# Kernel tuning notes

Measured on AMD Instinct MI355X. Metric: run time of the kernel, lower is better.

The kernel has to match this reference:

```python
import jax, jax.numpy as jnp
import numpy as np

N_NODES = 262144      # 2048 graphs * 128 nodes each
NUM_GRAPHS = 2048
MAX_NODES = 128
HIDDEN = 256
OUT_CH = 12
N_EDGES = 2097152     # ~avg degree 8


def setup_inputs() -> dict:
    key = jax.random.key(0)
    k1, k2, k3, k4 = jax.random.split(key, 4)
    x = jax.random.normal(k1, (N_NODES, HIDDEN), dtype=jnp.float32)
    # xavier-ish projection weight for Linear(6*hidden -> 12)
    W = jax.random.normal(k2, (OUT_CH, 6 * HIDDEN), dtype=jnp.float32) * (1.0 / np.sqrt(6 * HIDDEN))
    b = jnp.zeros((OUT_CH,), dtype=jnp.float32)
    # uniform graphs: sorted batch ids, MAX_NODES nodes per graph
    batch = (jnp.arange(N_NODES, dtype=jnp.int32) // MAX_NODES).astype(jnp.int32)
    # edges sampled within graphs: pick graph, then two local node ids
    g = jax.random.randint(k3, (N_EDGES,), 0, NUM_GRAPHS, dtype=jnp.int32)
    loc = jax.random.randint(k4, (N_EDGES, 2), 0, MAX_NODES, dtype=jnp.int32)
    src = g * MAX_NODES + loc[:, 0]
    dst = g * MAX_NODES + loc[:, 1]
    edge_index = jnp.stack([src, dst], axis=0).astype(jnp.int32)
    return {"x": x, "W": W, "b": b, "batch": batch, "edge_index": edge_index,
            "num_graphs": NUM_GRAPHS, "max_nodes": MAX_NODES}


def reference(x, W, b, batch, edge_index, num_graphs, max_nodes):
    N, H = x.shape
    G, M = num_graphs, max_nodes
    # local index of each node within its graph (batch is sorted by graph)
    counts = jax.ops.segment_sum(jnp.ones((N,), dtype=jnp.int32), batch, num_segments=G)
    starts = jnp.cumsum(counts) - counts            # exclusive prefix sum => first node of each graph
    local = jnp.arange(N, dtype=jnp.int32) - starts[batch]
    # dense per-graph node features X [G, M, H]
    X = jnp.zeros((G, M, H), dtype=x.dtype).at[batch, local].set(x)
    # dense symmetric adjacency A [G, M, M] (assignment semantics, like the torch loop)
    gi = batch[edge_index[0]]
    li = local[edge_index[0]]
    lj = local[edge_index[1]]
    A = jnp.zeros((G, M, M), dtype=x.dtype)
    A = A.at[gi, li, lj].set(1.0)
    A = A.at[gi, lj, li].set(1.0)
    # 6-gram walk readouts
    walk = X
    vs = [walk.sum(axis=1)]                          # v1
    for _ in range(5):                               # v2..v6
        walk = jnp.einsum('gnm,gmh->gnh', A, walk) * X
        vs.append(walk.sum(axis=1))
    out = jnp.concatenate(vs, axis=-1)               # == stack(dim=1).reshape(G, 6*H)
    out = out @ W.T + b                              # n_gram_projection
    return out
```

## Files before the change

### kernel.cpp

```cpp
#include <hip/hip_runtime.h>
#include <stdint.h>

#define NGRAPH 2048
#define MNODES 128
#define HID 256
#define OUTC 12
#define NEDGE 2097152

typedef __attribute__((ext_vector_type(8))) short short8;
typedef __attribute__((ext_vector_type(4))) float v4f;

#define SLICE 64
#define SWT_STRIDE 136

__device__ __forceinline__ unsigned short f2bf(float f) {
    unsigned int u = __builtin_bit_cast(unsigned int, f);
    u += 0x7fffu + ((u >> 16) & 1u);
    return (unsigned short)(u >> 16);
}

__global__ void build_bytes(const int* __restrict__ ei, unsigned char* __restrict__ Ab) {
    int e = blockIdx.x * blockDim.x + threadIdx.x;
    if (e >= NEDGE) return;
    int sN = ei[e];
    int dN = ei[NEDGE + e];
    int g = sN >> 7;
    int li = sN & 127;
    int lj = dN & 127;
    unsigned char* base = Ab + (size_t)g * (MNODES * MNODES);
    base[li * 128 + lj] = 1;
    base[lj * 128 + li] = 1;
}

__global__ void build_bits(const int* __restrict__ ei, unsigned int* __restrict__ bits) {
    int e = blockIdx.x * blockDim.x + threadIdx.x;
    if (e >= NEDGE) return;
    int sN = ei[e];
    int dN = ei[NEDGE + e];
    int g = sN >> 7;
    int li = sN & 127;
    int lj = dN & 127;
    unsigned int* base = bits + (size_t)g * (MNODES * 4);
    atomicOr(&base[li * 4 + (lj >> 5)], 1u << (lj & 31));
    atomicOr(&base[lj * 4 + (li >> 5)], 1u << (li & 31));
}

__launch_bounds__(256, 3)
__global__ void walk2(const float* __restrict__ x,
                      const float* __restrict__ W,
                      const unsigned char* __restrict__ Abytes,
                      const unsigned int* __restrict__ Abits,
                      int use_bytes,
                      float* __restrict__ partial) {
    __shared__ unsigned short sWT[SLICE][SWT_STRIDE];
    __shared__ float sVs2[2][6][SLICE];

    const int bx = blockIdx.x;
    const int g = bx >> 2;
    const int s = bx & 3;
    const int tid = threadIdx.x;
    const int wave = tid >> 6;
    const int lane = tid & 63;
    const int lrow = lane & 15;
    const int quad = lane >> 4;
    const int rhalf = wave >> 1;
    const int r0 = rhalf * 64;
    const int c0 = (wave & 1) * 32;
    const int cg0 = s * SLICE + c0;

    short8 areg[4][4];
    if (use_bytes) {
        const unsigned char* Ag = Abytes + (size_t)g * (MNODES * MNODES);
#pragma unroll
        for (int rt = 0; rt < 4; rt++) {
            int row = r0 + rt * 16 + lrow;
#pragma unroll
            for (int ks = 0; ks < 4; ks++) {
                int k0 = ks * 32 + quad * 8;
                uint2 u = *(const uint2*)(Ag + row * 128 + k0);
                short8 a;
#pragma unroll
                for (int j = 0; j < 8; j++) {
                    unsigned int byte = ((j < 4 ? u.x >> (8 * j) : u.y >> (8 * (j - 4))) & 0xFFu);
                    a[j] = (short)(byte ? 0x3F80 : 0);
                }
                areg[rt][ks] = a;
            }
        }
    } else {
        const unsigned int* Bg = Abits + (size_t)g * (MNODES * 4);
#pragma unroll
        for (int rt = 0; rt < 4; rt++) {
            int row = r0 + rt * 16 + lrow;
#pragma unroll
            for (int ks = 0; ks < 4; ks++) {
                unsigned int w = Bg[row * 4 + ks] >> (quad * 8);
                short8 a;
#pragma unroll
                for (int j = 0; j < 8; j++)
                    a[j] = (short)(((w >> j) & 1u) ? 0x3F80 : 0);
                areg[rt][ks] = a;
            }
        }
    }

    float xf[4][2][4];
    const float* xg = x + (size_t)g * (MNODES * HID);
#pragma unroll
    for (int rt = 0; rt < 4; rt++)
#pragma unroll
        for (int ct = 0; ct < 2; ct++) {
            int col = cg0 + ct * 16 + lrow;
#pragma unroll
            for (int reg = 0; reg < 4; reg++) {
                int row = r0 + rt * 16 + quad * 4 + reg;
                xf[rt][ct][reg] = xg[row * HID + col];
            }
        }
#pragma unroll
    for (int ct = 0; ct < 2; ct++) {
        int lcol = c0 + ct * 16 + lrow;
        float cs = 0.0f;
#pragma unroll
        for (int rt = 0; rt < 4; rt++) {
            int nbase = r0 + rt * 16 + quad * 4;
            uint2 u;
            u.x = (unsigned)f2bf(xf[rt][ct][0]) | ((unsigned)f2bf(xf[rt][ct][1]) << 16);
            u.y = (unsigned)f2bf(xf[rt][ct][2]) | ((unsigned)f2bf(xf[rt][ct][3]) << 16);
            *(uint2*)&sWT[lcol][nbase] = u;
            cs += xf[rt][ct][0] + xf[rt][ct][1] + xf[rt][ct][2] + xf[rt][ct][3];
        }
        cs += __shfl_xor(cs, 16);
        cs += __shfl_xor(cs, 32);
        if (quad == 0) sVs2[rhalf][0][lcol] = cs;
    }
    __syncthreads();

    for (int it = 1; it <= 5; it++) {
        v4f acc[4][2];
#pragma unroll
        for (int rt = 0; rt < 4; rt++)
#pragma unroll
            for (int ct = 0; ct < 2; ct++) acc[rt][ct] = (v4f)(0.0f);
#pragma unroll
        for (int ks = 0; ks < 4; ks++) {
            int k0 = ks * 32 + quad * 8;
#pragma unroll
            for (int ct = 0; ct < 2; ct++) {
                short8 bf = *(const short8*)&sWT[c0 + ct * 16 + lrow][k0];
#pragma unroll
                for (int rt = 0; rt < 4; rt++)
                    acc[rt][ct] = __builtin_amdgcn_mfma_f32_16x16x32_bf16(areg[rt][ks], bf, acc[rt][ct], 0, 0, 0);
            }
        }
        __syncthreads();
#pragma unroll
        for (int ct = 0; ct < 2; ct++) {
            int lcol = c0 + ct * 16 + lrow;
            float cs = 0.0f;
#pragma unroll
            for (int rt = 0; rt < 4; rt++) {
                float nw0 = acc[rt][ct][0] * xf[rt][ct][0];
                float nw1 = acc[rt][ct][1] * xf[rt][ct][1];
                float nw2 = acc[rt][ct][2] * xf[rt][ct][2];
                float nw3 = acc[rt][ct][3] * xf[rt][ct][3];
                int nbase = r0 + rt * 16 + quad * 4;
                uint2 u;
                u.x = (unsigned)f2bf(nw0) | ((unsigned)f2bf(nw1) << 16);
                u.y = (unsigned)f2bf(nw2) | ((unsigned)f2bf(nw3) << 16);
                *(uint2*)&sWT[lcol][nbase] = u;
                cs += nw0 + nw1 + nw2 + nw3;
            }
            cs += __shfl_xor(cs, 16);
            cs += __shfl_xor(cs, 32);
            if (quad == 0) sVs2[rhalf][it][lcol] = cs;
        }
        __syncthreads();
    }

    if (wave == 0) {
        for (int c = 0; c < OUTC; c++) {
            float p = 0.0f;
            const float* wr = W + c * (6 * HID);
#pragma unroll
            for (int ii = 0; ii < 6; ii++) {
                int i = ii * 64 + lane;
                int k = i >> 6;
                int h = i & 63;
                float v = sVs2[0][k][h] + sVs2[1][k][h];
                p += v * wr[k * HID + s * SLICE + h];
            }
#pragma unroll
            for (int off = 32; off >= 1; off >>= 1) p += __shfl_down(p, off);
            if (lane == 0) partial[bx * OUTC + c] = p;
        }
    }
}

__global__ void combine(const float* __restrict__ partial, const float* __restrict__ bvec,
                        float* __restrict__ out) {
    int i = blockIdx.x * blockDim.x + threadIdx.x;
    if (i >= NGRAPH * OUTC) return;
    int c = i % OUTC;
    int g = i / OUTC;
    float p = bvec[c];
#pragma unroll
    for (int s = 0; s < 4; s++) p += partial[(g * 4 + s) * OUTC + c];
    out[i] = p;
}

extern "C" void kernel_launch(void* const* d_in, const int* in_sizes, int n_in,
                              void* d_out, int out_size, void* d_ws, size_t ws_size,
                              hipStream_t stream) {
    const float* x = (const float*)d_in[0];
    const float* W = (const float*)d_in[1];
    const float* b = (const float*)d_in[2];
    const int* ei = (const int*)d_in[4];
    float* out = (float*)d_out;

    const size_t ABYTES = (size_t)NGRAPH * MNODES * MNODES;
    const size_t PARTIAL = (size_t)NGRAPH * 4 * OUTC * sizeof(float);

    if (ws_size >= ABYTES + PARTIAL) {
        unsigned char* Ab = (unsigned char*)d_ws;
        float* partial = (float*)((char*)d_ws + ABYTES);
        hipMemsetAsync(Ab, 0, ABYTES, stream);
        build_bytes<<<NEDGE / 256, 256, 0, stream>>>(ei, Ab);
        walk2<<<NGRAPH * 4, 256, 0, stream>>>(x, W, Ab, nullptr, 1, partial);
        combine<<<(NGRAPH * OUTC + 255) / 256, 256, 0, stream>>>(partial, b, out);
    } else {
        unsigned int* bits = (unsigned int*)d_ws;
        float* partial = (float*)((char*)d_ws + (size_t)NGRAPH * MNODES * 4 * 4);
        hipMemsetAsync(bits, 0, (size_t)NGRAPH * MNODES * 4 * 4, stream);
        build_bits<<<NEDGE / 512, 512, 0, stream>>>(ei, bits);
        walk2<<<NGRAPH * 4, 256, 0, stream>>>(x, W, nullptr, bits, 0, partial);
        combine<<<(NGRAPH * OUTC + 255) / 256, 256, 0, stream>>>(partial, b, out);
    }
}
```

Measured before the change: 507.3 us.

## Bucket edges per graph and build adjacency bitmaps in shared memory

Replaces the global dense byte adjacency matrix (memset plus scattered byte writes, then 16 KB of reads per block) with per-graph edge buckets. These are filled by an atomic slot counter, and each walk block then builds a 128x128 bitmap in LDS with atomicOr. The aim is to remove the large memset and the global adjacency traffic. The change also swaps the row padding of the LDS feature tile for an XOR swizzle, uses packed bf16 conversion intrinsics, and raises the occupancy hint to 4. The risks are contention on the 2048 global counters, and silently dropped edges for any graph with more than CAP=2048 edges.

Result: slower. 799.4 us (+57.6%).

```diff
diff --git a/kernel.cpp b/kernel.cpp
--- a/kernel.cpp
+++ b/kernel.cpp
@@ -1,58 +1,54 @@
 #include <hip/hip_runtime.h>
+#include <hip/hip_bf16.h>
 #include <stdint.h>
+#include <string.h>
 
 #define NGRAPH 2048
 #define MNODES 128
 #define HID 256
 #define OUTC 12
 #define NEDGE 2097152
+#define CAP 2048
+#define CNT_STRIDE 16
 
 typedef __attribute__((ext_vector_type(8))) short short8;
 typedef __attribute__((ext_vector_type(4))) float v4f;
 
 #define SLICE 64
-#define SWT_STRIDE 136
-
-__device__ __forceinline__ unsigned short f2bf(float f) {
-    unsigned int u = __builtin_bit_cast(unsigned int, f);
-    u += 0x7fffu + ((u >> 16) & 1u);
-    return (unsigned short)(u >> 16);
-}
-
-__global__ void build_bytes(const int* __restrict__ ei, unsigned char* __restrict__ Ab) {
+
+__device__ __forceinline__ int swz_off(int lcol, int kelem) {
+    int chunk = kelem >> 3;
+    int within = kelem & 7;
+    return (lcol << 7) + (((chunk ^ (lcol & 7)) << 3) | within);
+}
+
+__device__ __forceinline__ unsigned pk2(float a, float b) {
+    __hip_bfloat162 h = __float22bfloat162_rn(float2{a, b});
+    unsigned u;
+    memcpy(&u, &h, 4);
+    return u;
+}
+
+__global__ void scatter_edges(const int* __restrict__ ei, unsigned int* __restrict__ cnt,
+                              unsigned short* __restrict__ bucket) {
     int e = blockIdx.x * blockDim.x + threadIdx.x;
     if (e >= NEDGE) return;
     int sN = ei[e];
     int dN = ei[NEDGE + e];
     int g = sN >> 7;
-    int li = sN & 127;
-    int lj = dN & 127;
-    unsigned char* base = Ab + (size_t)g * (MNODES * MNODES);
-    base[li * 128 + lj] = 1;
-    base[lj * 128 + li] = 1;
-}
-
-__global__ void build_bits(const int* __restrict__ ei, unsigned int* __restrict__ bits) {
-    int e = blockIdx.x * blockDim.x + threadIdx.x;
-    if (e >= NEDGE) return;
-    int sN = ei[e];
-    int dN = ei[NEDGE + e];
-    int g = sN >> 7;
-    int li = sN & 127;
-    int lj = dN & 127;
-    unsigned int* base = bits + (size_t)g * (MNODES * 4);
-    atomicOr(&base[li * 4 + (lj >> 5)], 1u << (lj & 31));
-    atomicOr(&base[lj * 4 + (li >> 5)], 1u << (li & 31));
-}
-
-__launch_bounds__(256, 3)
-__global__ void walk2(const float* __restrict__ x,
+    unsigned short pk = (unsigned short)(((sN & 127) << 7) | (dN & 127));
+    unsigned slot = atomicAdd(&cnt[g * CNT_STRIDE], 1u);
+    if (slot < CAP) bucket[(size_t)g * CAP + slot] = pk;
+}
+
+__launch_bounds__(256, 4)
+__global__ void walk3(const float* __restrict__ x,
                       const float* __restrict__ W,
-                      const unsigned char* __restrict__ Abytes,
-                      const unsigned int* __restrict__ Abits,
-                      int use_bytes,
+                      const unsigned int* __restrict__ cnt,
+                      const unsigned short* __restrict__ bucket,
                       float* __restrict__ partial) {
-    __shared__ unsigned short sWT[SLICE][SWT_STRIDE];
+    __shared__ unsigned int sBits[MNODES * 4];
+    __shared__ unsigned short sWT[SLICE * 128];
     __shared__ float sVs2[2][6][SLICE];
 
     const int bx = blockIdx.x;
@@ -68,41 +64,8 @@
     const int c0 = (wave & 1) * 32;
     const int cg0 = s * SLICE + c0;
 
-    short8 areg[4][4];
-    if (use_bytes) {
-        const unsigned char* Ag = Abytes + (size_t)g * (MNODES * MNODES);
-#pragma unroll
-        for (int rt = 0; rt < 4; rt++) {
-            int row = r0 + rt * 16 + lrow;
-#pragma unroll
-            for (int ks = 0; ks < 4; ks++) {
-                int k0 = ks * 32 + quad * 8;
-                uint2 u = *(const uint2*)(Ag + row * 128 + k0);
-                short8 a;
-#pragma unroll
-                for (int j = 0; j < 8; j++) {
-                    unsigned int byte = ((j < 4 ? u.x >> (8 * j) : u.y >> (8 * (j - 4))) & 0xFFu);
-                    a[j] = (short)(byte ? 0x3F80 : 0);
-                }
-                areg[rt][ks] = a;
-            }
-        }
-    } else {
-        const unsigned int* Bg = Abits + (size_t)g * (MNODES * 4);
-#pragma unroll
-        for (int rt = 0; rt < 4; rt++) {
-            int row = r0 + rt * 16 + lrow;
-#pragma unroll
-            for (int ks = 0; ks < 4; ks++) {
-                unsigned int w = Bg[row * 4 + ks] >> (quad * 8);
-                short8 a;
-#pragma unroll
-                for (int j = 0; j < 8; j++)
-                    a[j] = (short)(((w >> j) & 1u) ? 0x3F80 : 0);
-                areg[rt][ks] = a;
-            }
-        }
-    }
+    sBits[tid] = 0u;
+    sBits[tid + 256] = 0u;
 
     float xf[4][2][4];
     const float* xg = x + (size_t)g * (MNODES * HID);
@@ -117,6 +80,33 @@
                 xf[rt][ct][reg] = xg[row * HID + col];
             }
         }
+
+    int ec = (int)min(cnt[g * CNT_STRIDE], (unsigned)CAP);
+    const unsigned short* bk = bucket + (size_t)g * CAP;
+    __syncthreads();
+    for (int e = tid; e < ec; e += 256) {
+        unsigned p = bk[e];
+        int li = p >> 7, lj = p & 127;
+        atomicOr(&sBits[li * 4 + (lj >> 5)], 1u << (lj & 31));
+        atomicOr(&sBits[lj * 4 + (li >> 5)], 1u << (li & 31));
+    }
+    __syncthreads();
+
+    short8 areg[4][4];
+#pragma unroll
+    for (int rt = 0; rt < 4; rt++) {
+        int row = r0 + rt * 16 + lrow;
+#pragma unroll
+        for (int ks = 0; ks < 4; ks++) {
+            unsigned w = sBits[row * 4 + ks] >> (quad * 8);
+            short8 a;
+#pragma unroll
+            for (int j = 0; j < 8; j++)
+                a[j] = (short)(((w >> j) & 1u) ? 0x3F80 : 0);
+            areg[rt][ks] = a;
+        }
+    }
+
 #pragma unroll
     for (int ct = 0; ct < 2; ct++) {
         int lcol = c0 + ct * 16 + lrow;
@@ -125,9 +115,9 @@
         for (int rt = 0; rt < 4; rt++) {
             int nbase = r0 + rt * 16 + quad * 4;
             uint2 u;
-            u.x = (unsigned)f2bf(xf[rt][ct][0]) | ((unsigned)f2bf(xf[rt][ct][1]) << 16);
-            u.y = (unsigned)f2bf(xf[rt][ct][2]) | ((unsigned)f2bf(xf[rt][ct][3]) << 16);
-            *(uint2*)&sWT[lcol][nbase] = u;
+            u.x = pk2(xf[rt][ct][0], xf[rt][ct][1]);
+            u.y = pk2(xf[rt][ct][2], xf[rt][ct][3]);
+            *(uint2*)&sWT[swz_off(lcol, nbase)] = u;
             cs += xf[rt][ct][0] + xf[rt][ct][1] + xf[rt][ct][2] + xf[rt][ct][3];
         }
         cs += __shfl_xor(cs, 16);
@@ -147,7 +137,7 @@
             int k0 = ks * 32 + quad * 8;
 #pragma unroll
             for (int ct = 0; ct < 2; ct++) {
-                short8 bf = *(const short8*)&sWT[c0 + ct * 16 + lrow][k0];
+                short8 bf = *(const short8*)&sWT[swz_off(c0 + ct * 16 + lrow, k0)];
 #pragma unroll
                 for (int rt = 0; rt < 4; rt++)
                     acc[rt][ct] = __builtin_amdgcn_mfma_f32_16x16x32_bf16(areg[rt][ks], bf, acc[rt][ct], 0, 0, 0);
@@ -166,9 +156,9 @@
                 float nw3 = acc[rt][ct][3] * xf[rt][ct][3];
                 int nbase = r0 + rt * 16 + quad * 4;
                 uint2 u;
-                u.x = (unsigned)f2bf(nw0) | ((unsigned)f2bf(nw1) << 16);
-                u.y = (unsigned)f2bf(nw2) | ((unsigned)f2bf(nw3) << 16);
-                *(uint2*)&sWT[lcol][nbase] = u;
+                u.x = pk2(nw0, nw1);
+                u.y = pk2(nw2, nw3);
+                *(uint2*)&sWT[swz_off(lcol, nbase)] = u;
                 cs += nw0 + nw1 + nw2 + nw3;
             }
             cs += __shfl_xor(cs, 16);
@@ -218,22 +208,15 @@
     const int* ei = (const int*)d_in[4];
     float* out = (float*)d_out;
 
-    const size_t ABYTES = (size_t)NGRAPH * MNODES * MNODES;
-    const size_t PARTIAL = (size_t)NGRAPH * 4 * OUTC * sizeof(float);
-
-    if (ws_size >= ABYTES + PARTIAL) {
-        unsigned char* Ab = (unsigned char*)d_ws;
-        float* partial = (float*)((char*)d_ws + ABYTES);
-        hipMemsetAsync(Ab, 0, ABYTES, stream);
-        build_bytes<<<NEDGE / 256, 256, 0, stream>>>(ei, Ab);
-        walk2<<<NGRAPH * 4, 256, 0, stream>>>(x, W, Ab, nullptr, 1, partial);
-        combine<<<(NGRAPH * OUTC + 255) / 256, 256, 0, stream>>>(partial, b, out);
-    } else {
-        unsigned int* bits = (unsigned int*)d_ws;
-        float* partial = (float*)((char*)d_ws + (size_t)NGRAPH * MNODES * 4 * 4);
-        hipMemsetAsync(bits, 0, (size_t)NGRAPH * MNODES * 4 * 4, stream);
-        build_bits<<<NEDGE / 512, 512, 0, stream>>>(ei, bits);
-        walk2<<<NGRAPH * 4, 256, 0, stream>>>(x, W, nullptr, bits, 0, partial);
-        combine<<<(NGRAPH * OUTC + 255) / 256, 256, 0, stream>>>(partial, b, out);
-    }
-}
+    const size_t CNT_BYTES = (size_t)NGRAPH * CNT_STRIDE * sizeof(unsigned int);
+    const size_t BKT_BYTES = (size_t)NGRAPH * CAP * sizeof(unsigned short);
+
+    unsigned int* cnt = (unsigned int*)d_ws;
+    unsigned short* bucket = (unsigned short*)((char*)d_ws + CNT_BYTES);
+    float* partial = (float*)((char*)d_ws + CNT_BYTES + BKT_BYTES);
+
+    (void)hipMemsetAsync(cnt, 0, CNT_BYTES, stream);
+    scatter_edges<<<NEDGE / 256, 256, 0, stream>>>(ei, cnt, bucket);
+    walk3<<<NGRAPH * 4, 256, 0, stream>>>(x, W, cnt, bucket, partial);
+    combine<<<(NGRAPH * OUTC + 255) / 256, 256, 0, stream>>>(partial, b, out);
+}
```
